# Kernel optimization log

Measured on AMD Instinct MI355X. Metric: run time of the kernel, lower is better.

Reference implementation:

```python
import jax, jax.numpy as jnp
import numpy as np

B, T, H, IN, D = 256, 64, 256, 2, 8

def _gru_cell(x, h, Wih, Whh, bih, bhh):
    gi = x @ Wih.T + bih          # [B,3H]
    gh = h @ Whh.T + bhh
    ir, iz, inn = jnp.split(gi, 3, axis=-1)
    hr, hz, hn = jnp.split(gh, 3, axis=-1)
    r = jax.nn.sigmoid(ir + hr)
    z = jax.nn.sigmoid(iz + hz)
    n = jnp.tanh(inn + r * hn)
    return (1.0 - z) * n + z * h

def _gru2(x, h, p):
    # h: [2,B,H]; p: 8-tuple of layer-0 then layer-1 GRU params
    h0 = _gru_cell(x, h[0], p[0], p[1], p[2], p[3])
    h1 = _gru_cell(h0, h[1], p[4], p[5], p[6], p[7])
    return jnp.stack([h0, h1], axis=0)

def _attend(h_new, buf, i, attn_W, v_W, fc_W, fc_b):
    # h_new: [2,B,H] fresh RNN hidden; buf: [B,T,2,H] history of hiddens
    s = h_new.transpose(1, 0, 2)                            # [B,2,H]
    es = jnp.einsum('blh,gh->blg', s, attn_W[:, :H])        # s half of cat(s,hiddens)
    eh = jnp.einsum('bjlh,gh->bjlg', buf, attn_W[:, H:])    # hiddens half
    energy = jnp.tanh(es[:, None] + eh)                     # [B,T,2,H]
    logits = jnp.einsum('bjlg,og->bjlo', energy, v_W)       # [B,T,2,2]
    mask = (jnp.arange(buf.shape[1]) <= i)[None, :, None, None]
    logits = jnp.where(mask, logits, jnp.float32(-1e30))
    m = logits.max(axis=(1, 2), keepdims=True)              # softmax over all 2*(i+1) history slots
    e = jnp.exp(logits - m)
    a = e / e.sum(axis=(1, 2), keepdims=True)
    c = jnp.einsum('bjlo,bjlh->obh', a, buf)                # [2,B,H] == bmm(a,hiddens).transpose(0,1)
    h_cat = jnp.concatenate([c, h_new], axis=-1)            # [2,B,2H]
    return h_cat @ fc_W.T + fc_b                            # [2,B,H]

def setup_inputs():
    key = jax.random.key(0)
    ks = jax.random.split(key, 32)
    def u(k, shape, fan):
        b = 1.0 / np.sqrt(fan)
        return jax.random.uniform(k, shape, jnp.float32, -b, b)
    inp = {'received': jax.random.normal(ks[0], (B, T, IN), jnp.float32)}
    i = 1
    for g in ('g1', 'g2'):
        inp[g + '_Wih0'] = u(ks[i], (3 * H, IN), H); i += 1
        inp[g + '_Whh0'] = u(ks[i], (3 * H, H), H); i += 1
        inp[g + '_bih0'] = u(ks[i], (3 * H,), H); i += 1
        inp[g + '_bhh0'] = u(ks[i], (3 * H,), H); i += 1
        inp[g + '_Wih1'] = u(ks[i], (3 * H, H), H); i += 1
        inp[g + '_Whh1'] = u(ks[i], (3 * H, H), H); i += 1
        inp[g + '_bih1'] = u(ks[i], (3 * H,), H); i += 1
        inp[g + '_bhh1'] = u(ks[i], (3 * H,), H); i += 1
    inp['fc_W'] = u(ks[i], (H, 2 * H), 2 * H); i += 1
    inp['fc_b'] = u(ks[i], (H,), 2 * H); i += 1
    inp['attn_W'] = u(ks[i], (H, 2 * H), 2 * H); i += 1
    inp['v_W'] = u(ks[i], (2, H), H); i += 1
    inp['out_W'] = u(ks[i], (1, 2 * H), 2 * H); i += 1
    inp['out_b'] = u(ks[i], (1,), 2 * H); i += 1
    return inp

def reference(received, g1_Wih0, g1_Whh0, g1_bih0, g1_bhh0, g1_Wih1, g1_Whh1, g1_bih1, g1_bhh1,
              g2_Wih0, g2_Whh0, g2_bih0, g2_bhh0, g2_Wih1, g2_Whh1, g2_bih1, g2_bhh1,
              fc_W, fc_b, attn_W, v_W, out_W, out_b):
    p1 = (g1_Wih0, g1_Whh0, g1_bih0, g1_bhh0, g1_Wih1, g1_Whh1, g1_bih1, g1_bhh1)
    p2 = (g2_Wih0, g2_Whh0, g2_bih0, g2_bhh0, g2_Wih1, g2_Whh1, g2_bih1, g2_bhh1)
    b, t = received.shape[0], received.shape[1]
    h_init = jnp.zeros((2, b, H), received.dtype)
    buf_init = jnp.zeros((b, t, 2, H), received.dtype)

    def step(carry, inp):
        h1, h2, b1, b2 = carry
        x, i = inp
        h1n = _gru2(x, h1, p1)
        h2n = _gru2(x, h2, p2)
        b1 = b1.at[:, i].set(h1n.transpose(1, 0, 2))
        b2 = b2.at[:, i].set(h2n.transpose(1, 0, 2))
        h1a = _attend(h1n, b1, i, attn_W, v_W, fc_W, fc_b)
        h2a = _attend(h2n, b2, i, attn_W, v_W, fc_W, fc_b)
        return (h1a, h2a, b1, b2), (h1n[1], h2n[1])

    xs = (received.transpose(1, 0, 2), jnp.arange(t))
    _, (o1, o2) = jax.lax.scan(step, (h_init, h_init, buf_init, buf_init), xs)
    out1 = o1.transpose(1, 0, 2)   # [B,T,H] = concat of per-step top-layer GRU outputs
    out2 = o2.transpose(1, 0, 2)
    ar = jnp.arange(t)
    idx = jnp.where(ar >= t - D - 1, t - 1, ar + D)   # delayed stream-2 features
    rnn_out = jnp.concatenate([out1, out2[:, idx]], axis=-1)  # [B,T,2H]
    return jax.nn.sigmoid(rnn_out @ out_W.T + out_b)          # [B,T,1]
```

## Files before the change

kernel.cpp:

```cpp
#include <hip/hip_runtime.h>

#define BATCH 256
#define TT    64
#define HH    256
#define DD    8

#define BW    4
#define NTHR  1024
#define NBLK  (2 * (BATCH / BW))

typedef __attribute__((ext_vector_type(8))) short bfrag;
typedef __attribute__((ext_vector_type(4))) float f4;
typedef __attribute__((ext_vector_type(4))) unsigned int uv4;
typedef __attribute__((ext_vector_type(2))) unsigned int uv2;

#define SWZ(g) ((((g) & 31) << 3) | ((g) >> 5))

__device__ __forceinline__ float rcpf(float x) { return __builtin_amdgcn_rcpf(x); }
__device__ __forceinline__ float sigf(float x) { return rcpf(1.0f + __expf(-x)); }
__device__ __forceinline__ float tanh_fast(float x) {
  const float e = __expf(-2.0f * x);
  return __builtin_fmaf(2.0f, rcpf(1.0f + e), -1.0f);
}
__device__ __forceinline__ unsigned short f2bf(float f) {
  union { float f; unsigned int u; } v; v.f = f;
  return (unsigned short)((v.u + 0x7fffu + ((v.u >> 16) & 1u)) >> 16);
}
__device__ __forceinline__ float bf_lo(unsigned int u) {
  union { unsigned int u; float f; } v; v.u = u << 16; return v.f;
}
__device__ __forceinline__ float bf_hi(unsigned int u) {
  union { unsigned int u; float f; } v; v.u = u & 0xffff0000u; return v.f;
}
__device__ __forceinline__ bfrag zero_frag() {
  bfrag r;
#pragma unroll
  for (int x = 0; x < 8; x++) r[x] = 0;
  return r;
}
__device__ __forceinline__ f4 mfma16(bfrag a, bfrag b, f4 c) {
  return __builtin_amdgcn_mfma_f32_16x16x32_bf16(a, b, c, 0, 0, 0);
}

#define W1_ELEMS  196608
#define STACK_W   (3 * W1_ELEMS)
#define B3_OFF    (2 * STACK_W)
#define B4_OFF    (B3_OFF + 131072)
#define WF_TOTAL  (B4_OFF + 131072)

__global__ __launch_bounds__(256) void prep_weights(
    const float* __restrict__ g1_Whh0, const float* __restrict__ g1_Wih1, const float* __restrict__ g1_Whh1,
    const float* __restrict__ g2_Whh0, const float* __restrict__ g2_Wih1, const float* __restrict__ g2_Whh1,
    const float* __restrict__ attn_W, const float* __restrict__ fc_W,
    unsigned short* __restrict__ wf) {
  const int id = blockIdx.x * 256 + threadIdx.x;
  if (id >= WF_TOTAL) return;
  float src;
  if (id < 2 * STACK_W) {
    const int s = id / STACK_W, r = id % STACK_W;
    const int mm = r / W1_ELEMS, e = r % W1_ELEMS;
    const int j = e & 7, lane = (e >> 3) & 63, c = (e >> 9) & 7, t = e >> 12;
    const int nt = t / 3, g = t % 3;
    const int n = nt * 16 + (lane & 15);
    const int k = c * 32 + ((lane >> 4) << 3) + j;
    const float* W = (mm == 0) ? (s ? g2_Whh0 : g1_Whh0)
                   : (mm == 1) ? (s ? g2_Wih1 : g1_Wih1)
                               : (s ? g2_Whh1 : g1_Whh1);
    src = W[(g * 256 + n) * 256 + k];
  } else if (id < B4_OFF) {
    const int e = id - B3_OFF;
    const int j = e & 7, lane = (e >> 3) & 63, c = (e >> 9) & 7, t = e >> 12;
    const int n = t * 16 + (lane & 15);
    const int k = c * 32 + ((lane >> 4) << 3) + j;
    src = (n < 256) ? attn_W[n * 512 + k] : attn_W[(n - 256) * 512 + 256 + k];
  } else {
    const int e = id - B4_OFF;
    const int j = e & 7, lane = (e >> 3) & 63, c = (e >> 9) & 15, t = e >> 13;
    const int n = t * 16 + (lane & 15);
    const int k = c * 32 + ((lane >> 4) << 3) + j;
    src = fc_W[n * 512 + k];
  }
  wf[id] = f2bf(src);
}

__global__ __launch_bounds__(NTHR, 4) void gru_attn(
    const float* __restrict__ received,
    const float* __restrict__ g1_Wih0, const float* __restrict__ g1_bih0, const float* __restrict__ g1_bhh0,
    const float* __restrict__ g1_bih1, const float* __restrict__ g1_bhh1,
    const float* __restrict__ g2_Wih0, const float* __restrict__ g2_bih0, const float* __restrict__ g2_bhh0,
    const float* __restrict__ g2_bih1, const float* __restrict__ g2_bhh1,
    const float* __restrict__ fc_b, const float* __restrict__ v_W, const float* __restrict__ out_W,
    const unsigned short* __restrict__ wf,
    unsigned short* __restrict__ buf_g, unsigned short* __restrict__ ehb_g,
    float* __restrict__ ws_p) {
  const int tid  = threadIdx.x;
  const int lane = tid & 63, wave = tid >> 6;
  const int col  = lane & 15, q = lane >> 4;
  const int s    = blockIdx.x & 1;
  const int b0   = (blockIdx.x >> 1) * BW;

  const float* Wih0 = s ? g2_Wih0 : g1_Wih0;
  const float* bih0 = s ? g2_bih0 : g1_bih0;
  const float* bhh0 = s ? g2_bhh0 : g1_bhh0;
  const float* bih1 = s ? g2_bih1 : g1_bih1;
  const float* bhh1 = s ? g2_bhh1 : g1_bhh1;

  const bfrag* W1  = (const bfrag*)(wf + (size_t)s * STACK_W);
  const bfrag* W2I = W1 + W1_ELEMS / 8;
  const bfrag* W2H = W2I + W1_ELEMS / 8;
  const bfrag* B3  = (const bfrag*)(wf + B3_OFF);
  const bfrag* B4  = (const bfrag*)(wf + B4_OFF);

  unsigned short* buf = buf_g + (size_t)s * BATCH * TT * 2 * HH;
  unsigned short* ehb = ehb_g + (size_t)s * BATCH * TT * 2 * HH;
  float* pp = ws_p + (size_t)s * BATCH * TT;

  const int nm0 = wave * 16 + col;
  const float wxr0 = Wih0[nm0 * 2],         wxr1 = Wih0[nm0 * 2 + 1];
  const float wxz0 = Wih0[(256 + nm0) * 2], wxz1 = Wih0[(256 + nm0) * 2 + 1];
  const float wxn0 = Wih0[(512 + nm0) * 2], wxn1 = Wih0[(512 + nm0) * 2 + 1];
  const float br0  = bih0[nm0] + bhh0[nm0];
  const float bz0  = bih0[256 + nm0] + bhh0[256 + nm0];
  const float bni0 = bih0[512 + nm0], bnh0 = bhh0[512 + nm0];
  const float br1  = bih1[nm0] + bhh1[nm0];
  const float bz1  = bih1[256 + nm0] + bhh1[256 + nm0];
  const float bni1 = bih1[512 + nm0], bnh1 = bhh1[512 + nm0];
  const float fcb  = fc_b[nm0];
  const float owv  = out_W[s * HH + nm0];

  __shared__ float          hf[8 * 260] __attribute__((aligned(16)));
  __shared__ unsigned short hb[8 * 264] __attribute__((aligned(16)));
  __shared__ unsigned short hnb[8 * 264] __attribute__((aligned(16)));
  __shared__ float          es_s[8 * 264] __attribute__((aligned(16)));
  __shared__ unsigned short cacb[8 * 264] __attribute__((aligned(16)));
  __shared__ float          lp[TT * 4 * 2 * 2];
  __shared__ float          vw_s[512];
  __shared__ float          cpart[4 * 2 * 4 * 256] __attribute__((aligned(16)));
  __shared__ float          pw_s[64];
  __shared__ float          sinv_s[8];

  for (int x = tid; x < 8 * 260; x += NTHR) hf[x] = 0.0f;
  for (int x = tid; x < 8 * 264; x += NTHR) hb[x] = 0;
  if (tid < 512) { const int o = tid >> 8, g = tid & 255; vw_s[o * 256 + SWZ(g)] = v_W[tid]; }
  __syncthreads();

#pragma unroll 1
  for (int i = 0; i < TT; ++i) {
    float2 xv[BW];
#pragma unroll
    for (int b = 0; b < BW; b++) xv[b] = ((const float2*)received)[(size_t)(b0 + b) * TT + i];

    {
      bfrag a0[8];
#pragma unroll
      for (int c = 0; c < 8; c++)
        a0[c] = (col < BW) ? *(const bfrag*)&hb[col * 264 + c * 32 + q * 8] : zero_frag();
      const int nt16 = wave;
      bfrag bb[24];
#pragma unroll
      for (int c = 0; c < 8; c++) {
        bb[c]      = W1[((nt16 * 3 + 0) * 8 + c) * 64 + lane];
        bb[8 + c]  = W1[((nt16 * 3 + 1) * 8 + c) * 64 + lane];
        bb[16 + c] = W1[((nt16 * 3 + 2) * 8 + c) * 64 + lane];
      }
      f4 aR = {0, 0, 0, 0}, aZ = {0, 0, 0, 0}, aN = {0, 0, 0, 0};
#pragma unroll
      for (int c = 0; c < 8; c++) {
        aR = mfma16(a0[c], bb[c], aR);
        aZ = mfma16(a0[c], bb[8 + c], aZ);
        aN = mfma16(a0[c], bb[16 + c], aN);
      }
      if (lane < 16) {
#pragma unroll
        for (int reg = 0; reg < 4; reg++) {
          const int b = reg;
          const float rr = sigf(xv[b].x * wxr0 + xv[b].y * wxr1 + br0 + aR[reg]);
          const float zz = sigf(xv[b].x * wxz0 + xv[b].y * wxz1 + bz0 + aZ[reg]);
          const float nn = tanh_fast(xv[b].x * wxn0 + xv[b].y * wxn1 + bni0 +
                                     rr * (aN[reg] + bnh0));
          const float hn0 = (1.0f - zz) * nn + zz * hf[b * 260 + nm0];
          const unsigned short hv = f2bf(hn0);
          hnb[b * 264 + nm0] = hv;
          buf[((size_t)(b0 + b) * (TT * 2) + i * 2 + 0) * HH + nm0] = hv;
        }
      }
    }
    __syncthreads();

    {
      bfrag ai[8], ah[8];
#pragma unroll
      for (int c = 0; c < 8; c++) {
        ai[c] = (col < BW) ? *(const bfrag*)&hnb[col * 264 + c * 32 + q * 8] : zero_frag();
        ah[c] = (col < BW) ? *(const bfrag*)&hb[(4 + col) * 264 + c * 32 + q * 8] : zero_frag();
      }
      float pv[4] = {0.f, 0.f, 0.f, 0.f};
      const int nt16 = wave;
      bfrag bb[24];
#pragma unroll
      for (int c = 0; c < 8; c++) {
        bb[c]      = W2I[((nt16 * 3 + 0) * 8 + c) * 64 + lane];
        bb[8 + c]  = W2I[((nt16 * 3 + 1) * 8 + c) * 64 + lane];
        bb[16 + c] = W2I[((nt16 * 3 + 2) * 8 + c) * 64 + lane];
      }
      f4 iR = {0, 0, 0, 0}, iZ = {0, 0, 0, 0}, iN = {0, 0, 0, 0};
#pragma unroll
      for (int c = 0; c < 8; c++) {
        iR = mfma16(ai[c], bb[c], iR);
        iZ = mfma16(ai[c], bb[8 + c], iZ);
        iN = mfma16(ai[c], bb[16 + c], iN);
      }
#pragma unroll
      for (int c = 0; c < 8; c++) {
        bb[c]      = W2H[((nt16 * 3 + 0) * 8 + c) * 64 + lane];
        bb[8 + c]  = W2H[((nt16 * 3 + 1) * 8 + c) * 64 + lane];
        bb[16 + c] = W2H[((nt16 * 3 + 2) * 8 + c) * 64 + lane];
      }
      f4 hR = {0, 0, 0, 0}, hZ = {0, 0, 0, 0}, hN = {0, 0, 0, 0};
#pragma unroll
      for (int c = 0; c < 8; c++) {
        hR = mfma16(ah[c], bb[c], hR);
        hZ = mfma16(ah[c], bb[8 + c], hZ);
        hN = mfma16(ah[c], bb[16 + c], hN);
      }
      if (lane < 16) {
#pragma unroll
        for (int reg = 0; reg < 4; reg++) {
          const int b = reg;
          const float rr = sigf(iR[reg] + hR[reg] + br1);
          const float zz = sigf(iZ[reg] + hZ[reg] + bz1);
          const float nn = tanh_fast(iN[reg] + bni1 + rr * (hN[reg] + bnh1));
          const float hn1 = (1.0f - zz) * nn + zz * hf[(4 + b) * 260 + nm0];
          const unsigned short hv = f2bf(hn1);
          hnb[(4 + b) * 264 + nm0] = hv;
          buf[((size_t)(b0 + b) * (TT * 2) + i * 2 + 1) * HH + nm0] = hv;
          pv[reg] += hn1 * owv;
        }
      }
#pragma unroll
      for (int reg = 0; reg < 4; reg++) {
#pragma unroll
        for (int d = 1; d < 16; d <<= 1) pv[reg] += __shfl_xor(pv[reg], d, 64);
      }
      if (lane == 0) {
#pragma unroll
        for (int reg = 0; reg < 4; reg++) pw_s[wave * 4 + reg] = pv[reg];
      }
    }
    __syncthreads();

    {
      bfrag a3[8];
#pragma unroll
      for (int c = 0; c < 8; c++)
        a3[c] = (col < 8) ? *(const bfrag*)&hnb[col * 264 + c * 32 + q * 8] : zero_frag();
#pragma unroll
      for (int tt = 0; tt < 2; tt++) {
        const int t = wave * 2 + tt;
        bfrag bb[8];
#pragma unroll
        for (int c = 0; c < 8; c++) bb[c] = B3[(t * 8 + c) * 64 + lane];
        f4 acc = {0, 0, 0, 0};
#pragma unroll
        for (int c = 0; c < 8; c++) acc = mfma16(a3[c], bb[c], acc);
        if (lane < 32) {
          const int n = t * 16 + col;
#pragma unroll
          for (int reg = 0; reg < 4; reg++) {
            const int m = q * 4 + reg;
            const int l = m >> 2, b = m & 3;
            if (t < 16) es_s[(b * 2 + l) * 264 + SWZ(n)] = acc[reg];
            else ehb[((size_t)(b0 + b) * (TT * 2) + i * 2 + l) * HH + (n - 256)] = f2bf(acc[reg]);
          }
        }
      }
      if (tid < 4) {
        float ss = 0.0f;
#pragma unroll
        for (int w = 0; w < 16; w++) ss += pw_s[w * 4 + tid];
        pp[(size_t)(b0 + tid) * TT + i] = ss;
      }
    }
    __syncthreads();

    {
      const int nslot = 64 * (i + 1);
      int slot = tid;
      uv4 cur[4];
      if (slot < nslot) {
        const uv4* ep = (const uv4*)(ehb + ((size_t)(b0 + ((slot >> 3) & 3)) * (TT * 2) +
                                            (slot >> 6) * 2 + ((slot >> 5) & 1)) * HH + (slot & 7) * 32);
#pragma unroll
        for (int u = 0; u < 4; u++) cur[u] = __builtin_nontemporal_load(ep + u);
      }
      for (; slot < nslot; slot += NTHR) {
        const int snext = slot + NTHR;
        uv4 nxt[4];
        if (snext < nslot) {
          const uv4* ep2 = (const uv4*)(ehb + ((size_t)(b0 + ((snext >> 3) & 3)) * (TT * 2) +
                                               (snext >> 6) * 2 + ((snext >> 5) & 1)) * HH + (snext & 7) * 32);
#pragma unroll
          for (int u = 0; u < 4; u++) nxt[u] = __builtin_nontemporal_load(ep2 + u);
        } else {
#pragma unroll
          for (int u = 0; u < 4; u++) nxt[u] = cur[u];
        }
        const int g8 = slot & 7;
        const int b  = (slot >> 3) & 3;
        const int l  = (slot >> 5) & 1;
        const int j  = slot >> 6;
        const int eb = (b * 2 + l) * 264;
        float l0 = 0.0f, l1 = 0.0f;
#pragma unroll
        for (int u = 0; u < 4; u++) {
#pragma unroll
          for (int k = 0; k < 4; k++) {
            const int m = u * 8 + k * 2;
            const float e0 = tanh_fast(es_s[eb + (m * 8 + g8)] + bf_lo(cur[u][k]));
            const float e1 = tanh_fast(es_s[eb + ((m + 1) * 8 + g8)] + bf_hi(cur[u][k]));
            l0 = fmaf(e0, vw_s[m * 8 + g8], fmaf(e1, vw_s[(m + 1) * 8 + g8], l0));
            l1 = fmaf(e0, vw_s[256 + m * 8 + g8], fmaf(e1, vw_s[256 + (m + 1) * 8 + g8], l1));
          }
        }
#pragma unroll
        for (int d = 1; d < 8; d <<= 1) { l0 += __shfl_xor(l0, d, 64); l1 += __shfl_xor(l1, d, 64); }
        if (g8 == 0) {
          lp[((j * 4 + b) * 2 + l) * 2 + 0] = __expf(l0);
          lp[((j * 4 + b) * 2 + l) * 2 + 1] = __expf(l1);
        }
#pragma unroll
        for (int u = 0; u < 4; u++) cur[u] = nxt[u];
      }
    }
    __syncthreads();

    {
      if (wave < 8) {
        const int b = wave >> 1, o = wave & 1;
        const int jl2 = 2 * (i + 1);
        const int jl0 = lane, jl1 = lane + 64;
        float sa = 0.0f;
        if (jl0 < jl2) sa += lp[((jl0 >> 1) * 4 + b) * 4 + (jl0 & 1) * 2 + o];
        if (jl1 < jl2) sa += lp[((jl1 >> 1) * 4 + b) * 4 + (jl1 & 1) * 2 + o];
#pragma unroll
        for (int d = 1; d < 64; d <<= 1) sa += __shfl_xor(sa, d, 64);
        if (lane == 0) sinv_s[b * 2 + o] = rcpf(sa);
      }
      const int h4   = tid & 63;
      const int jpar = (tid >> 6) & 3;
      const int cb   = tid >> 8;
      const uv2* bp = (const uv2*)(buf + ((size_t)(b0 + cb) * (TT * 2)) * HH);
      float c00 = 0.f, c01 = 0.f, c02 = 0.f, c03 = 0.f;
      float c10 = 0.f, c11 = 0.f, c12 = 0.f, c13 = 0.f;
      uv2 aj0 = {0, 0}, aj1 = {0, 0}, bj0 = {0, 0}, bj1 = {0, 0};
      int j = jpar;
      if (j <= i) {
        aj0 = __builtin_nontemporal_load(bp + (j * 2 + 0) * 64 + h4);
        aj1 = __builtin_nontemporal_load(bp + (j * 2 + 1) * 64 + h4);
        bj0 = __builtin_nontemporal_load(bp + ((j + 4) * 2 + 0) * 64 + h4);
        bj1 = __builtin_nontemporal_load(bp + ((j + 4) * 2 + 1) * 64 + h4);
      }
      for (; j <= i; j += 4) {
        uv2 cj0 = {0, 0}, cj1 = {0, 0};
        if (j + 8 <= i) {
          cj0 = __builtin_nontemporal_load(bp + ((j + 8) * 2 + 0) * 64 + h4);
          cj1 = __builtin_nontemporal_load(bp + ((j + 8) * 2 + 1) * 64 + h4);
        }
#pragma unroll
        for (int l = 0; l < 2; l++) {
          const uv2 u = l ? aj1 : aj0;
          const float e0 = lp[((j * 4 + cb) * 2 + l) * 2 + 0];
          const float e1 = lp[((j * 4 + cb) * 2 + l) * 2 + 1];
          const float v0 = bf_lo(u[0]), v1 = bf_hi(u[0]);
          const float v2 = bf_lo(u[1]), v3 = bf_hi(u[1]);
          c00 = fmaf(e0, v0, c00); c01 = fmaf(e0, v1, c01);
          c02 = fmaf(e0, v2, c02); c03 = fmaf(e0, v3, c03);
          c10 = fmaf(e1, v0, c10); c11 = fmaf(e1, v1, c11);
          c12 = fmaf(e1, v2, c12); c13 = fmaf(e1, v3, c13);
        }
        aj0 = bj0; aj1 = bj1; bj0 = cj0; bj1 = cj1;
      }
      ((float4*)&cpart[((jpar * 2 + 0) * 4 + cb) * 256])[h4] = make_float4(c00, c01, c02, c03);
      ((float4*)&cpart[((jpar * 2 + 1) * 4 + cb) * 256])[h4] = make_float4(c10, c11, c12, c13);
    }
    __syncthreads();

    for (int x = tid; x < 2 * BW * HH; x += NTHR) {
      const int g = x & 255, b = (x >> 8) & 3, o = x >> 10;
      const float v = (cpart[((0 * 2 + o) * 4 + b) * 256 + g] +
                       cpart[((1 * 2 + o) * 4 + b) * 256 + g] +
                       cpart[((2 * 2 + o) * 4 + b) * 256 + g] +
                       cpart[((3 * 2 + o) * 4 + b) * 256 + g]) *
                      sinv_s[b * 2 + o];
      cacb[(o * 4 + b) * 264 + g] = f2bf(v);
    }
    __syncthreads();

    {
      bfrag a4[16];
      if (col < 8) {
#pragma unroll
        for (int c = 0; c < 8; c++) {
          a4[c]     = *(const bfrag*)&cacb[col * 264 + c * 32 + q * 8];
          a4[c + 8] = *(const bfrag*)&hnb[col * 264 + c * 32 + q * 8];
        }
      } else {
#pragma unroll
        for (int c = 0; c < 16; c++) a4[c] = zero_frag();
      }
      const int t16 = wave;
      bfrag bb[16];
#pragma unroll
      for (int c = 0; c < 16; c++) bb[c] = B4[(t16 * 16 + c) * 64 + lane];
      f4 acc = {0, 0, 0, 0};
#pragma unroll
      for (int c = 0; c < 16; c++) acc = mfma16(a4[c], bb[c], acc);
      if (lane < 32) {
#pragma unroll
        for (int reg = 0; reg < 4; reg++) {
          const int m = q * 4 + reg;
          const float v = acc[reg] + fcb;
          hf[m * 260 + nm0] = v;
          hb[m * 264 + nm0] = f2bf(v);
        }
      }
    }
    __syncthreads();
  }
}

__global__ __launch_bounds__(256) void final_combine(const float* __restrict__ ws_p,
                                                     const float* __restrict__ out_b,
                                                     float* __restrict__ out) {
  const int gidx = blockIdx.x * blockDim.x + threadIdx.x;
  if (gidx >= BATCH * TT) return;
  const int b = gidx >> 6;
  const int t = gidx & 63;
  const int idx = (t >= TT - DD - 1) ? (TT - 1) : (t + DD);
  const float* p1 = ws_p;
  const float* p2 = ws_p + (size_t)BATCH * TT;
  const float v = p1[(size_t)b * TT + t] + p2[(size_t)b * TT + idx] + out_b[0];
  out[gidx] = 1.0f / (1.0f + __expf(-v));
}

extern "C" void kernel_launch(void* const* d_in, const int* in_sizes, int n_in,
                              void* d_out, int out_size, void* d_ws, size_t ws_size,
                              hipStream_t stream) {
  const float* received = (const float*)d_in[0];
  const float* g1_Wih0 = (const float*)d_in[1];
  const float* g1_Whh0 = (const float*)d_in[2];
  const float* g1_bih0 = (const float*)d_in[3];
  const float* g1_bhh0 = (const float*)d_in[4];
  const float* g1_Wih1 = (const float*)d_in[5];
  const float* g1_Whh1 = (const float*)d_in[6];
  const float* g1_bih1 = (const float*)d_in[7];
  const float* g1_bhh1 = (const float*)d_in[8];
  const float* g2_Wih0 = (const float*)d_in[9];
  const float* g2_Whh0 = (const float*)d_in[10];
  const float* g2_bih0 = (const float*)d_in[11];
  const float* g2_bhh0 = (const float*)d_in[12];
  const float* g2_Wih1 = (const float*)d_in[13];
  const float* g2_Whh1 = (const float*)d_in[14];
  const float* g2_bih1 = (const float*)d_in[15];
  const float* g2_bhh1 = (const float*)d_in[16];
  const float* fc_W   = (const float*)d_in[17];
  const float* fc_b   = (const float*)d_in[18];
  const float* attn_W = (const float*)d_in[19];
  const float* v_W    = (const float*)d_in[20];
  const float* out_W  = (const float*)d_in[21];
  const float* out_b  = (const float*)d_in[22];

  float* ws_p = (float*)d_ws;
  unsigned short* buf = (unsigned short*)(ws_p + 2 * BATCH * TT);
  unsigned short* ehb = buf + (size_t)2 * BATCH * TT * 2 * HH;
  unsigned short* wf  = ehb + (size_t)2 * BATCH * TT * 2 * HH;

  hipLaunchKernelGGL(prep_weights, dim3((WF_TOTAL + 255) / 256), dim3(256), 0, stream,
                     g1_Whh0, g1_Wih1, g1_Whh1, g2_Whh0, g2_Wih1, g2_Whh1,
                     attn_W, fc_W, wf);

  hipLaunchKernelGGL(gru_attn, dim3(NBLK), dim3(NTHR), 0, stream,
                     received,
                     g1_Wih0, g1_bih0, g1_bhh0, g1_bih1, g1_bhh1,
                     g2_Wih0, g2_bih0, g2_bhh0, g2_bih1, g2_bhh1,
                     fc_b, v_W, out_W, wf, buf, ehb, ws_p);

  hipLaunchKernelGGL(final_combine, dim3((BATCH * TT + 255) / 256), dim3(256), 0, stream,
                     ws_p, out_b, (float*)d_out);
}
```

Measured before the change: 5.618 ms.

## Process eight batch rows per block to fill MFMA rows and halve blocks

Each block now owns eight batch rows instead of four, so the number of blocks halves. The 16-row MFMA tiles, which were mostly zero padding, now hold eight rows per layer in the GRU step and sixteen in the attention and fc steps. Every weight fragment fetched per step therefore serves twice as many rows, cutting total weight traffic from L2. All index maps, shared buffers and the context reduction are remapped to match. In exchange, each block does more serial work per timestep in the softmax and context loops (two j-partitions instead of four), and the smaller grid spreads the latency-bound recurrence over fewer CUs.

```diff
diff --git a/kernel.cpp b/kernel.cpp
--- a/kernel.cpp
+++ b/kernel.cpp
@@ -5,7 +5,7 @@
 #define HH    256
 #define DD    8
 
-#define BW    4
+#define BW    8
 #define NTHR  1024
 #define NBLK  (2 * (BATCH / BW))
 
@@ -128,27 +128,30 @@
   const float fcb  = fc_b[nm0];
   const float owv  = out_W[s * HH + nm0];
 
-  __shared__ float          hf[8 * 260] __attribute__((aligned(16)));
-  __shared__ unsigned short hb[8 * 264] __attribute__((aligned(16)));
-  __shared__ unsigned short hnb[8 * 264] __attribute__((aligned(16)));
-  __shared__ float          es_s[8 * 264] __attribute__((aligned(16)));
-  __shared__ unsigned short cacb[8 * 264] __attribute__((aligned(16)));
-  __shared__ float          lp[TT * 4 * 2 * 2];
+  __shared__ float          hf[16 * 260] __attribute__((aligned(16)));
+  __shared__ unsigned short hb[16 * 264] __attribute__((aligned(16)));
+  __shared__ unsigned short hnb[16 * 264] __attribute__((aligned(16)));
+  __shared__ float          es_s[16 * 264] __attribute__((aligned(16)));
+  __shared__ unsigned short cacb[16 * 264] __attribute__((aligned(16)));
+  __shared__ float          lp[TT * 8 * 2 * 2];
   __shared__ float          vw_s[512];
-  __shared__ float          cpart[4 * 2 * 4 * 256] __attribute__((aligned(16)));
-  __shared__ float          pw_s[64];
-  __shared__ float          sinv_s[8];
-
-  for (int x = tid; x < 8 * 260; x += NTHR) hf[x] = 0.0f;
-  for (int x = tid; x < 8 * 264; x += NTHR) hb[x] = 0;
+  __shared__ float          cpart[2 * 2 * 8 * 256] __attribute__((aligned(16)));
+  __shared__ float          pw_s[16 * 8];
+  __shared__ float          sinv_s[16];
+
+  for (int x = tid; x < 16 * 260; x += NTHR) hf[x] = 0.0f;
+  for (int x = tid; x < 16 * 264; x += NTHR) hb[x] = 0;
   if (tid < 512) { const int o = tid >> 8, g = tid & 255; vw_s[o * 256 + SWZ(g)] = v_W[tid]; }
   __syncthreads();
 
 #pragma unroll 1
   for (int i = 0; i < TT; ++i) {
-    float2 xv[BW];
-#pragma unroll
-    for (int b = 0; b < BW; b++) xv[b] = ((const float2*)received)[(size_t)(b0 + b) * TT + i];
+    float2 xq[4] = {};
+    if (lane < 32) {
+#pragma unroll
+      for (int reg = 0; reg < 4; reg++)
+        xq[reg] = ((const float2*)received)[(size_t)(b0 + q * 4 + reg) * TT + i];
+    }
 
     {
       bfrag a0[8];
@@ -170,13 +173,13 @@
         aZ = mfma16(a0[c], bb[8 + c], aZ);
         aN = mfma16(a0[c], bb[16 + c], aN);
       }
-      if (lane < 16) {
+      if (lane < 32) {
 #pragma unroll
         for (int reg = 0; reg < 4; reg++) {
-          const int b = reg;
-          const float rr = sigf(xv[b].x * wxr0 + xv[b].y * wxr1 + br0 + aR[reg]);
-          const float zz = sigf(xv[b].x * wxz0 + xv[b].y * wxz1 + bz0 + aZ[reg]);
-          const float nn = tanh_fast(xv[b].x * wxn0 + xv[b].y * wxn1 + bni0 +
+          const int b = q * 4 + reg;
+          const float rr = sigf(xq[reg].x * wxr0 + xq[reg].y * wxr1 + br0 + aR[reg]);
+          const float zz = sigf(xq[reg].x * wxz0 + xq[reg].y * wxz1 + bz0 + aZ[reg]);
+          const float nn = tanh_fast(xq[reg].x * wxn0 + xq[reg].y * wxn1 + bni0 +
                                      rr * (aN[reg] + bnh0));
           const float hn0 = (1.0f - zz) * nn + zz * hf[b * 260 + nm0];
           const unsigned short hv = f2bf(hn0);
@@ -192,7 +195,7 @@
 #pragma unroll
       for (int c = 0; c < 8; c++) {
         ai[c] = (col < BW) ? *(const bfrag*)&hnb[col * 264 + c * 32 + q * 8] : zero_frag();
-        ah[c] = (col < BW) ? *(const bfrag*)&hb[(4 + col) * 264 + c * 32 + q * 8] : zero_frag();
+        ah[c] = (col < BW) ? *(const bfrag*)&hb[(8 + col) * 264 + c * 32 + q * 8] : zero_frag();
       }
       float pv[4] = {0.f, 0.f, 0.f, 0.f};
       const int nt16 = wave;
@@ -223,16 +226,16 @@
         hZ = mfma16(ah[c], bb[8 + c], hZ);
         hN = mfma16(ah[c], bb[16 + c], hN);
       }
-      if (lane < 16) {
+      if (lane < 32) {
 #pragma unroll
         for (int reg = 0; reg < 4; reg++) {
-          const int b = reg;
+          const int b = q * 4 + reg;
           const float rr = sigf(iR[reg] + hR[reg] + br1);
           const float zz = sigf(iZ[reg] + hZ[reg] + bz1);
           const float nn = tanh_fast(iN[reg] + bni1 + rr * (hN[reg] + bnh1));
-          const float hn1 = (1.0f - zz) * nn + zz * hf[(4 + b) * 260 + nm0];
+          const float hn1 = (1.0f - zz) * nn + zz * hf[(8 + b) * 260 + nm0];
           const unsigned short hv = f2bf(hn1);
-          hnb[(4 + b) * 264 + nm0] = hv;
+          hnb[(8 + b) * 264 + nm0] = hv;
           buf[((size_t)(b0 + b) * (TT * 2) + i * 2 + 1) * HH + nm0] = hv;
           pv[reg] += hn1 * owv;
         }
@@ -242,9 +245,9 @@
 #pragma unroll
         for (int d = 1; d < 16; d <<= 1) pv[reg] += __shfl_xor(pv[reg], d, 64);
       }
-      if (lane == 0) {
-#pragma unroll
-        for (int reg = 0; reg < 4; reg++) pw_s[wave * 4 + reg] = pv[reg];
+      if (col == 0 && q < 2) {
+#pragma unroll
+        for (int reg = 0; reg < 4; reg++) pw_s[wave * 8 + q * 4 + reg] = pv[reg];
       }
     }
     __syncthreads();
@@ -253,7 +256,7 @@
       bfrag a3[8];
 #pragma unroll
       for (int c = 0; c < 8; c++)
-        a3[c] = (col < 8) ? *(const bfrag*)&hnb[col * 264 + c * 32 + q * 8] : zero_frag();
+        a3[c] = *(const bfrag*)&hnb[col * 264 + c * 32 + q * 8];
 #pragma unroll
       for (int tt = 0; tt < 2; tt++) {
         const int t = wave * 2 + tt;
@@ -263,33 +266,33 @@
         f4 acc = {0, 0, 0, 0};
 #pragma unroll
         for (int c = 0; c < 8; c++) acc = mfma16(a3[c], bb[c], acc);
-        if (lane < 32) {
+        {
           const int n = t * 16 + col;
 #pragma unroll
           for (int reg = 0; reg < 4; reg++) {
             const int m = q * 4 + reg;
-            const int l = m >> 2, b = m & 3;
+            const int l = m >> 3, b = m & 7;
             if (t < 16) es_s[(b * 2 + l) * 264 + SWZ(n)] = acc[reg];
             else ehb[((size_t)(b0 + b) * (TT * 2) + i * 2 + l) * HH + (n - 256)] = f2bf(acc[reg]);
           }
         }
       }
-      if (tid < 4) {
+      if (tid < 8) {
         float ss = 0.0f;
 #pragma unroll
-        for (int w = 0; w < 16; w++) ss += pw_s[w * 4 + tid];
+        for (int w = 0; w < 16; w++) ss += pw_s[w * 8 + tid];
         pp[(size_t)(b0 + tid) * TT + i] = ss;
       }
     }
     __syncthreads();
 
     {
-      const int nslot = 64 * (i + 1);
+      const int nslot = 128 * (i + 1);
       int slot = tid;
       uv4 cur[4];
       if (slot < nslot) {
-        const uv4* ep = (const uv4*)(ehb + ((size_t)(b0 + ((slot >> 3) & 3)) * (TT * 2) +
-                                            (slot >> 6) * 2 + ((slot >> 5) & 1)) * HH + (slot & 7) * 32);
+        const uv4* ep = (const uv4*)(ehb + ((size_t)(b0 + ((slot >> 3) & 7)) * (TT * 2) +
+                                            (slot >> 7) * 2 + ((slot >> 6) & 1)) * HH + (slot & 7) * 32);
 #pragma unroll
         for (int u = 0; u < 4; u++) cur[u] = __builtin_nontemporal_load(ep + u);
       }
@@ -297,8 +300,8 @@
         const int snext = slot + NTHR;
         uv4 nxt[4];
         if (snext < nslot) {
-          const uv4* ep2 = (const uv4*)(ehb + ((size_t)(b0 + ((snext >> 3) & 3)) * (TT * 2) +
-                                               (snext >> 6) * 2 + ((snext >> 5) & 1)) * HH + (snext & 7) * 32);
+          const uv4* ep2 = (const uv4*)(ehb + ((size_t)(b0 + ((snext >> 3) & 7)) * (TT * 2) +
+                                               (snext >> 7) * 2 + ((snext >> 6) & 1)) * HH + (snext & 7) * 32);
 #pragma unroll
           for (int u = 0; u < 4; u++) nxt[u] = __builtin_nontemporal_load(ep2 + u);
         } else {
@@ -306,9 +309,9 @@
           for (int u = 0; u < 4; u++) nxt[u] = cur[u];
         }
         const int g8 = slot & 7;
-        const int b  = (slot >> 3) & 3;
-        const int l  = (slot >> 5) & 1;
-        const int j  = slot >> 6;
+        const int b  = (slot >> 3) & 7;
+        const int l  = (slot >> 6) & 1;
+        const int j  = slot >> 7;
         const int eb = (b * 2 + l) * 264;
         float l0 = 0.0f, l1 = 0.0f;
 #pragma unroll
@@ -325,8 +328,8 @@
 #pragma unroll
         for (int d = 1; d < 8; d <<= 1) { l0 += __shfl_xor(l0, d, 64); l1 += __shfl_xor(l1, d, 64); }
         if (g8 == 0) {
-          lp[((j * 4 + b) * 2 + l) * 2 + 0] = __expf(l0);
-          lp[((j * 4 + b) * 2 + l) * 2 + 1] = __expf(l1);
+          lp[((j * 8 + b) * 2 + l) * 2 + 0] = __expf(l0);
+          lp[((j * 8 + b) * 2 + l) * 2 + 1] = __expf(l1);
         }
 #pragma unroll
         for (int u = 0; u < 4; u++) cur[u] = nxt[u];
@@ -335,20 +338,20 @@
     __syncthreads();
 
     {
-      if (wave < 8) {
+      {
         const int b = wave >> 1, o = wave & 1;
         const int jl2 = 2 * (i + 1);
         const int jl0 = lane, jl1 = lane + 64;
         float sa = 0.0f;
-        if (jl0 < jl2) sa += lp[((jl0 >> 1) * 4 + b) * 4 + (jl0 & 1) * 2 + o];
-        if (jl1 < jl2) sa += lp[((jl1 >> 1) * 4 + b) * 4 + (jl1 & 1) * 2 + o];
+        if (jl0 < jl2) sa += lp[((jl0 >> 1) * 8 + b) * 4 + (jl0 & 1) * 2 + o];
+        if (jl1 < jl2) sa += lp[((jl1 >> 1) * 8 + b) * 4 + (jl1 & 1) * 2 + o];
 #pragma unroll
         for (int d = 1; d < 64; d <<= 1) sa += __shfl_xor(sa, d, 64);
         if (lane == 0) sinv_s[b * 2 + o] = rcpf(sa);
       }
       const int h4   = tid & 63;
-      const int jpar = (tid >> 6) & 3;
-      const int cb   = tid >> 8;
+      const int jpar = (tid >> 6) & 1;
+      const int cb   = tid >> 7;
       const uv2* bp = (const uv2*)(buf + ((size_t)(b0 + cb) * (TT * 2)) * HH);
       float c00 = 0.f, c01 = 0.f, c02 = 0.f, c03 = 0.f;
       float c10 = 0.f, c11 = 0.f, c12 = 0.f, c13 = 0.f;
@@ -357,20 +360,20 @@
       if (j <= i) {
         aj0 = __builtin_nontemporal_load(bp + (j * 2 + 0) * 64 + h4);
         aj1 = __builtin_nontemporal_load(bp + (j * 2 + 1) * 64 + h4);
-        bj0 = __builtin_nontemporal_load(bp + ((j + 4) * 2 + 0) * 64 + h4);
-        bj1 = __builtin_nontemporal_load(bp + ((j + 4) * 2 + 1) * 64 + h4);
-      }
-      for (; j <= i; j += 4) {
+        bj0 = __builtin_nontemporal_load(bp + ((j + 2) * 2 + 0) * 64 + h4);
+        bj1 = __builtin_nontemporal_load(bp + ((j + 2) * 2 + 1) * 64 + h4);
+      }
+      for (; j <= i; j += 2) {
         uv2 cj0 = {0, 0}, cj1 = {0, 0};
-        if (j + 8 <= i) {
-          cj0 = __builtin_nontemporal_load(bp + ((j + 8) * 2 + 0) * 64 + h4);
-          cj1 = __builtin_nontemporal_load(bp + ((j + 8) * 2 + 1) * 64 + h4);
+        if (j + 4 <= i) {
+          cj0 = __builtin_nontemporal_load(bp + ((j + 4) * 2 + 0) * 64 + h4);
+          cj1 = __builtin_nontemporal_load(bp + ((j + 4) * 2 + 1) * 64 + h4);
         }
 #pragma unroll
         for (int l = 0; l < 2; l++) {
           const uv2 u = l ? aj1 : aj0;
-          const float e0 = lp[((j * 4 + cb) * 2 + l) * 2 + 0];
-          const float e1 = lp[((j * 4 + cb) * 2 + l) * 2 + 1];
+          const float e0 = lp[((j * 8 + cb) * 2 + l) * 2 + 0];
+          const float e1 = lp[((j * 8 + cb) * 2 + l) * 2 + 1];
           const float v0 = bf_lo(u[0]), v1 = bf_hi(u[0]);
           const float v2 = bf_lo(u[1]), v3 = bf_hi(u[1]);
           c00 = fmaf(e0, v0, c00); c01 = fmaf(e0, v1, c01);
@@ -380,33 +383,26 @@
         }
         aj0 = bj0; aj1 = bj1; bj0 = cj0; bj1 = cj1;
       }
-      ((float4*)&cpart[((jpar * 2 + 0) * 4 + cb) * 256])[h4] = make_float4(c00, c01, c02, c03);
-      ((float4*)&cpart[((jpar * 2 + 1) * 4 + cb) * 256])[h4] = make_float4(c10, c11, c12, c13);
+      ((float4*)&cpart[((jpar * 2 + 0) * 8 + cb) * 256])[h4] = make_float4(c00, c01, c02, c03);
+      ((float4*)&cpart[((jpar * 2 + 1) * 8 + cb) * 256])[h4] = make_float4(c10, c11, c12, c13);
     }
     __syncthreads();
 
     for (int x = tid; x < 2 * BW * HH; x += NTHR) {
-      const int g = x & 255, b = (x >> 8) & 3, o = x >> 10;
-      const float v = (cpart[((0 * 2 + o) * 4 + b) * 256 + g] +
-                       cpart[((1 * 2 + o) * 4 + b) * 256 + g] +
-                       cpart[((2 * 2 + o) * 4 + b) * 256 + g] +
-                       cpart[((3 * 2 + o) * 4 + b) * 256 + g]) *
+      const int g = x & 255, b = (x >> 8) & 7, o = x >> 11;
+      const float v = (cpart[((0 * 2 + o) * 8 + b) * 256 + g] +
+                       cpart[((1 * 2 + o) * 8 + b) * 256 + g]) *
                       sinv_s[b * 2 + o];
-      cacb[(o * 4 + b) * 264 + g] = f2bf(v);
+      cacb[(o * 8 + b) * 264 + g] = f2bf(v);
     }
     __syncthreads();
 
     {
       bfrag a4[16];
-      if (col < 8) {
-#pragma unroll
-        for (int c = 0; c < 8; c++) {
-          a4[c]     = *(const bfrag*)&cacb[col * 264 + c * 32 + q * 8];
-          a4[c + 8] = *(const bfrag*)&hnb[col * 264 + c * 32 + q * 8];
-        }
-      } else {
-#pragma unroll
-        for (int c = 0; c < 16; c++) a4[c] = zero_frag();
+#pragma unroll
+      for (int c = 0; c < 8; c++) {
+        a4[c]     = *(const bfrag*)&cacb[col * 264 + c * 32 + q * 8];
+        a4[c + 8] = *(const bfrag*)&hnb[col * 264 + c * 32 + q * 8];
       }
       const int t16 = wave;
       bfrag bb[16];
@@ -415,7 +411,7 @@
       f4 acc = {0, 0, 0, 0};
 #pragma unroll
       for (int c = 0; c < 16; c++) acc = mfma16(a4[c], bb[c], acc);
-      if (lane < 32) {
+      {
 #pragma unroll
         for (int reg = 0; reg < 4; reg++) {
           const int m = q * 4 + reg;
```

Result: slower. 6.572 ms (+17.0%).
